# Optimization experiments

Measured on AMD Instinct MI355X. Metric: run time of the kernel, lower is better.

Reference implementation:

```python
import jax, jax.numpy as jnp
import numpy as np

# Static video grid (F, H, W); S = F*H*W tokens.
F_FRAMES, H_GRID, W_GRID = 9, 16, 28
DIM, N_HEADS = 1536, 12
HEAD_DIM = DIM // N_HEADS          # 128
ROT = HEAD_DIM // 2                # 64 complex pairs
EPS = 1e-6


def setup_inputs() -> dict:
    key = jax.random.key(0)
    ks = jax.random.split(key, 12)
    S = F_FRAMES * H_GRID * W_GRID
    scale = 0.02
    inp = {
        "x": jax.random.normal(ks[0], (1, S, DIM), jnp.float32),
        "seq_lens": jnp.array([S], jnp.int32),
        "grid_sizes": jnp.array([[F_FRAMES, H_GRID, W_GRID]], jnp.int32),
        "freqs": jax.random.normal(ks[1], (1024, ROT), jnp.float32),  # rope angles
        "Wq": jax.random.normal(ks[2], (DIM, DIM), jnp.float32) * scale,
        "bq": jnp.zeros((DIM,), jnp.float32),
        "Wk": jax.random.normal(ks[3], (DIM, DIM), jnp.float32) * scale,
        "bk": jnp.zeros((DIM,), jnp.float32),
        "Wv": jax.random.normal(ks[4], (DIM, DIM), jnp.float32) * scale,
        "bv": jnp.zeros((DIM,), jnp.float32),
        "Wo": jax.random.normal(ks[5], (DIM, DIM), jnp.float32) * scale,
        "bo": jnp.zeros((DIM,), jnp.float32),
        "gq": jnp.ones((DIM,), jnp.float32),
        "gk": jnp.ones((DIM,), jnp.float32),
    }
    return inp


def _rms_norm(h, g):
    # WanRMSNorm: h * rsqrt(mean(h^2) + eps) * weight
    var = jnp.mean(jnp.square(h), axis=-1, keepdims=True)
    return h * jax.lax.rsqrt(var + EPS) * g


def _rope_angles(freqs):
    # Split channel dim into temporal / height / width parts.
    c = ROT
    t_dim = c - 2 * (c // 3)  # 22
    s1 = c // 3               # 21
    temporal, height, width = freqs[:, :t_dim], freqs[:, t_dim:t_dim + s1], freqs[:, t_dim + s1:]
    t_ang = jnp.repeat(temporal[:F_FRAMES], H_GRID * W_GRID, axis=0)         # [S, 22]
    h_ang = jnp.tile(jnp.repeat(height[:H_GRID], W_GRID, axis=0), (F_FRAMES, 1))  # [S, 21]
    w_ang = jnp.tile(jnp.tile(width[:W_GRID], (H_GRID, 1)), (F_FRAMES, 1))        # [S, 21]
    return jnp.concatenate([t_ang, h_ang, w_ang], axis=-1)  # [S, c]


def _rope_apply(x, ang):
    # x: [B, S, n, d] viewed as complex pairs [B, S, n, d/2, 2]
    b, s, n, d = x.shape
    xp = x.reshape(b, s, n, d // 2, 2)
    xr, xi = xp[..., 0], xp[..., 1]
    cos = jnp.cos(ang)[None, :, None, :]
    sin = jnp.sin(ang)[None, :, None, :]
    out_r = xr * cos - xi * sin
    out_i = xr * sin + xi * cos
    return jnp.stack([out_r, out_i], axis=-1).reshape(b, s, n, d)


def reference(x, seq_lens, grid_sizes, freqs, Wq, bq, Wk, bk, Wv, bv, Wo, bo, gq, gk):
    b, s, _ = x.shape
    n, d = N_HEADS, HEAD_DIM
    q = _rms_norm(x @ Wq + bq, gq).reshape(b, s, n, d)
    k = _rms_norm(x @ Wk + bk, gk).reshape(b, s, n, d)
    v = (x @ Wv + bv).reshape(b, s, n, d)

    ang = _rope_angles(freqs)  # [S, d/2]
    rq = _rope_apply(q, ang)
    rk = _rope_apply(k, ang)

    # Causal frame-block mask: query in frame i attends to kv in frames <= i.
    frame_idx = jnp.arange(s) // (H_GRID * W_GRID)
    mask = frame_idx[None, :] <= frame_idx[:, None]  # [S_q, S_k]

    scale = 1.0 / jnp.sqrt(jnp.asarray(d, x.dtype))
    scores = jnp.einsum("bqnd,bknd->bnqk", rq, rk) * scale
    scores = jnp.where(mask[None, None], scores, jnp.asarray(-1e30, scores.dtype))
    probs = jax.nn.softmax(scores, axis=-1)
    attn = jnp.einsum("bnqk,bknd->bqnd", probs, v).reshape(b, s, n * d)
    return attn @ Wo + bo
```

## Files before the change

kernel.cpp:

```cpp
#include <hip/hip_runtime.h>
#include <stdint.h>

typedef unsigned short u16;
typedef unsigned int u32;
typedef __attribute__((ext_vector_type(8))) short bf16x8;
typedef __attribute__((ext_vector_type(4))) float f32x4;

#define S_LEN 4032
#define S_PAD 4096
#define DIMC  1536
#define HD    128
#define FRAME 448

static const size_t OFF_FLAG  = 0;
static const size_t OFF_CANON = 256;
static const size_t OFF_XB    = 524288;
static const size_t OFF_WT    = OFF_XB  + 12582912;
static const size_t OFF_WOT   = OFF_WT  + 14155776;
static const size_t OFF_YQ    = OFF_WOT + 4718592;
static const size_t OFF_YK    = OFF_YQ  + 12582912;
static const size_t OFF_VT    = OFF_YK  + 12582912;
static const size_t OFF_QH    = OFF_VT  + 12582912;
static const size_t OFF_KH    = OFF_QH  + 12386304;
static const size_t OFF_AT    = OFF_KH  + 12386304;
static const size_t WS_NEED   = OFF_AT  + 12582912;

#define C_BQ 0
#define C_BO 4608
#define C_GQ 6144
#define C_GK 7680
#define C_FR 9216
#define C_TOT 74752

__device__ __forceinline__ u16 f2bf(float f) {
  union { float f; u32 u; } v; v.f = f;
  u32 u = v.u;
  u32 r = (u + 0x7fffu + ((u >> 16) & 1u)) >> 16;
  return (u16)r;
}
__device__ __forceinline__ float bf2f(u16 h) {
  union { float f; u32 u; } v; v.u = ((u32)h) << 16;
  return v.f;
}

__device__ __forceinline__ void gld_lds16(const void* g, void* l) {
  __builtin_amdgcn_global_load_lds(
      (const __attribute__((address_space(1))) void*)(uintptr_t)g,
      (__attribute__((address_space(3))) void*)(u32)(uintptr_t)l,
      16, 0, 0);
}

__device__ __forceinline__ f32x4 mfma16(bf16x8 a, bf16x8 b, f32x4 c) {
  return __builtin_amdgcn_mfma_f32_16x16x32_bf16(a, b, c, 0, 0, 0);
}

__global__ void prep_all(const void* __restrict__ x,
                         const void* Wq, const void* Wk, const void* Wv, const void* Wo,
                         const void* bq, const void* bk, const void* bv, const void* bo,
                         const void* gq, const void* gk, const void* fr,
                         float* __restrict__ canon, u16* __restrict__ xb,
                         u16* __restrict__ wqkvt, u16* __restrict__ wot,
                         int* __restrict__ flag) {
  __shared__ int cnt;
  __shared__ float tile[32][33];
  const int tid = threadIdx.x;
  if (tid == 0) cnt = 0;
  __syncthreads();
  int e = (((const u16*)x)[2 * tid] >> 7) & 0xff;
  if (e > 150) atomicAdd(&cnt, 1);
  __syncthreads();
  const int fl = (cnt >= 8) ? 1 : 0;
  const int bid = blockIdx.x;
  if (bid == 0 && tid == 0) *flag = fl;

  if (bid < 9216) {
    const int z = bid / 2304;
    const int rem = bid % 2304;
    const int by = rem / 48, bx = rem % 48;
    const void* W = (z == 0) ? Wq : (z == 1) ? Wk : (z == 2) ? Wv : Wo;
    u16* dst = (z < 3) ? (wqkvt + (size_t)z * DIMC * DIMC) : wot;
    const int tx = tid & 31, ty = tid >> 5;
    const int c = bx * 32 + tx;
    #pragma unroll
    for (int i = 0; i < 4; i++) {
      int r = by * 32 + ty + i * 8;
      float v = fl ? ((const float*)W)[(size_t)r * DIMC + c]
                   : bf2f(((const u16*)W)[(size_t)r * DIMC + c]);
      tile[ty + i * 8][tx] = v;
    }
    __syncthreads();
    const int k = by * 32 + tx;
    #pragma unroll
    for (int i = 0; i < 4; i++) {
      int n = bx * 32 + ty + i * 8;
      dst[(size_t)n * DIMC + k] = f2bf(tile[tx][ty + i * 8]);
    }
  } else if (bid < 12288) {
    int i = (bid - 9216) * 256 + tid;
    if (i < (S_PAD * DIMC) / 8) {
      size_t base = (size_t)i * 8;
      int row = (int)(base / DIMC);
      union { u16 h[8]; uint4 v; } u;
      if (row < S_LEN) {
        if (fl) {
          const float* xf = (const float*)x + base;
          #pragma unroll
          for (int j = 0; j < 8; j++) u.h[j] = f2bf(xf[j]);
        } else {
          const u16* xh = (const u16*)x + base;
          #pragma unroll
          for (int j = 0; j < 8; j++) u.h[j] = xh[j];
        }
      } else {
        #pragma unroll
        for (int j = 0; j < 8; j++) u.h[j] = 0;
      }
      ((uint4*)xb)[i] = u.v;
    }
  } else {
    for (int i = (bid - 12288) * 256 + tid; i < C_TOT; i += 292 * 256) {
      const void* src; int j;
      if      (i < 1536) { src = bq; j = i; }
      else if (i < 3072) { src = bk; j = i - 1536; }
      else if (i < 4608) { src = bv; j = i - 3072; }
      else if (i < 6144) { src = bo; j = i - 4608; }
      else if (i < 7680) { src = gq; j = i - 6144; }
      else if (i < 9216) { src = gk; j = i - 7680; }
      else               { src = fr; j = i - 9216; }
      canon[i] = fl ? ((const float*)src)[j] : bf2f(((const u16*)src)[j]);
    }
  }
}

template <int MODE>
__launch_bounds__(256, 4)
__global__ void gemm_bt(const u16* __restrict__ A, const u16* __restrict__ Bt,
                        const float* __restrict__ canon,
                        u16* __restrict__ Yq, u16* __restrict__ Yk, u16* __restrict__ Vt,
                        void* __restrict__ Out, const int* __restrict__ flagp) {
  const int bm0 = blockIdx.y * 128, bn0 = blockIdx.x * 128;
  const int tid = threadIdx.x, wave = tid >> 6, lane = tid & 63;
  const int wm = wave >> 1, wn = wave & 1;
  const int l15 = lane & 15, l4 = lane >> 4;
  __shared__ u16 sA[128 * 64];
  __shared__ u16 sB[128 * 64];
  f32x4 acc[4][4];
  #pragma unroll
  for (int i = 0; i < 4; i++)
    #pragma unroll
    for (int j = 0; j < 4; j++) acc[i][j] = (f32x4){0.f, 0.f, 0.f, 0.f};

  const int swc = ((lane & 7) ^ (lane >> 3)) * 8;
  const u16* Ab = A  + (size_t)(bm0 + (lane >> 3)) * DIMC + swc;
  const u16* Bb = Bt + (size_t)(bn0 + (lane >> 3)) * DIMC + swc;

  for (int kt = 0; kt < DIMC; kt += 64) {
    __syncthreads();
    #pragma unroll
    for (int c = 0; c < 4; c++) {
      int g = wave * 4 + c;
      gld_lds16(Ab + (size_t)g * 8 * DIMC + kt, (char*)sA + g * 1024);
      gld_lds16(Bb + (size_t)g * 8 * DIMC + kt, (char*)sB + g * 1024);
    }
    __syncthreads();
    #pragma unroll
    for (int ks = 0; ks < 2; ks++) {
      bf16x8 av[4], bvv[4];
      #pragma unroll
      for (int mt = 0; mt < 4; mt++)
        av[mt]  = *(const bf16x8*)(sA + (wm * 64 + mt * 16 + l15) * 64 +
                                   (((ks * 4 + l4) ^ (l15 & 7)) * 8));
      #pragma unroll
      for (int nt = 0; nt < 4; nt++)
        bvv[nt] = *(const bf16x8*)(sB + (wn * 64 + nt * 16 + l15) * 64 +
                                   (((ks * 4 + l4) ^ (l15 & 7)) * 8));
      #pragma unroll
      for (int mt = 0; mt < 4; mt++)
        #pragma unroll
        for (int nt = 0; nt < 4; nt++)
          acc[mt][nt] = mfma16(av[mt], bvv[nt], acc[mt][nt]);
    }
  }

  const int gm0 = bm0 + wm * 64;
  const int gn0 = bn0 + wn * 64;
  if (MODE == 0) {
    #pragma unroll
    for (int nt = 0; nt < 4; nt++) {
      int gn = gn0 + nt * 16 + l15;
      float b = canon[C_BQ + gn];
      #pragma unroll
      for (int mt = 0; mt < 4; mt++) {
        int gm = gm0 + mt * 16 + l4 * 4;
        if (gn < 1536) {
          #pragma unroll
          for (int r = 0; r < 4; r++)
            Yq[(size_t)(gm + r) * DIMC + gn] = f2bf(acc[mt][nt][r] + b);
        } else if (gn < 3072) {
          int g2 = gn - 1536;
          #pragma unroll
          for (int r = 0; r < 4; r++)
            Yk[(size_t)(gm + r) * DIMC + g2] = f2bf(acc[mt][nt][r] + b);
        } else {
          int g2 = gn - 3072;
          u32 lo = (u32)f2bf(acc[mt][nt][0] + b) | ((u32)f2bf(acc[mt][nt][1] + b) << 16);
          u32 hi = (u32)f2bf(acc[mt][nt][2] + b) | ((u32)f2bf(acc[mt][nt][3] + b) << 16);
          uint2 pk; pk.x = lo; pk.y = hi;
          *(uint2*)(Vt + (size_t)g2 * S_PAD + gm) = pk;
        }
      }
    }
  } else {
    const int fl = *flagp;
    #pragma unroll
    for (int nt = 0; nt < 4; nt++) {
      int gn = gn0 + nt * 16 + l15;
      float b = canon[C_BO + gn];
      #pragma unroll
      for (int mt = 0; mt < 4; mt++) {
        int gm = gm0 + mt * 16 + l4 * 4;
        #pragma unroll
        for (int r = 0; r < 4; r++) {
          int gr = gm + r;
          if (gr < S_LEN) {
            float v = acc[mt][nt][r] + b;
            if (fl) ((float*)Out)[(size_t)gr * DIMC + gn] = v;
            else    ((u16*)Out)[(size_t)gr * DIMC + gn] = f2bf(v);
          }
        }
      }
    }
  }
}

__global__ void norm_rope(const u16* __restrict__ Yq, const u16* __restrict__ Yk,
                          const float* __restrict__ canon, u16* __restrict__ Qh,
                          u16* __restrict__ Kh) {
  const int tid = threadIdx.x, wave = tid >> 6, lane = tid & 63;
  const int s = blockIdx.x * 4 + wave;
  const int isq = (blockIdx.y == 0);
  const u16* Y = isq ? Yq : Yk;
  const float* g = canon + (isq ? C_GQ : C_GK);
  u16* Oh = isq ? Qh : Kh;
  const float sc = isq ? (0.08838834764831845f * 1.4426950408889634f) : 1.0f;

  const u32* yrow = (const u32*)Y + (size_t)s * 768;
  float xr[12], xi[12];
  float ss = 0.f;
  #pragma unroll
  for (int i = 0; i < 12; i++) {
    u32 d = yrow[lane + 64 * i];
    float a = bf2f((u16)(d & 0xffff));
    float b = bf2f((u16)(d >> 16));
    xr[i] = a; xi[i] = b;
    ss += a * a + b * b;
  }
  #pragma unroll
  for (int dd = 1; dd < 64; dd <<= 1) ss += __shfl_xor(ss, dd, 64);
  float rms = rsqrtf(ss * (1.f / 1536.f) + 1e-6f);

  int f_ = s / FRAME, hh = (s % FRAME) / 28, ww = s % 28;
  const float* fr = canon + C_FR;
  float a = (lane < 22) ? fr[f_ * 64 + lane]
          : (lane < 43) ? fr[hh * 64 + lane]
                        : fr[ww * 64 + lane];
  float si, co;
  __sincosf(a, &si, &co);

  const float2* g2 = (const float2*)g;
  #pragma unroll
  for (int i = 0; i < 12; i++) {
    int p = lane + 64 * i;
    float2 gg = g2[p];
    float r  = xr[i] * rms * gg.x;
    float im = xi[i] * rms * gg.y;
    u32 pk = (u32)f2bf((r * co - im * si) * sc) | ((u32)f2bf((r * si + im * co) * sc) << 16);
    ((u32*)Oh)[((size_t)i * S_LEN + s) * 64 + lane] = pk;
  }
}

__launch_bounds__(256, 4)
__global__ void attn_v7(const u16* __restrict__ Qh, const u16* __restrict__ Kh,
                        const u16* __restrict__ Vt, u16* __restrict__ Ab) {
  const int tid = threadIdx.x, wave = tid >> 6, lane = tid & 63;
  const int l15 = lane & 15, l4 = lane >> 4;
  const int h = blockIdx.x % 12;
  const int qb = 62 - (blockIdx.x / 12);
  const int q0 = qb * 64;
  const int nkv = (q0 / FRAME + 1) * 7;
  __shared__ u16 sK[8192];
  __shared__ u16 sV[8192];
  __shared__ u16 sP[4][1024];

  int koff[4], voff[4];
  #pragma unroll
  for (int i = 0; i < 4; i++) {
    int c = i * 256 + tid;
    int r = c >> 4, cc = (c & 15) ^ (r & 15);
    koff[i] = r * HD + cc * 8;
    int rv = c >> 3, cv = (c & 7) ^ (rv & 7);
    voff[i] = rv * S_PAD + cv * 8;
  }

  bf16x8 qf[4];
  {
    const u16* qp = Qh + ((size_t)h * S_LEN + q0 + wave * 16 + l15) * HD + l4 * 8;
    #pragma unroll
    for (int ks = 0; ks < 4; ks++) qf[ks] = *(const bf16x8*)(qp + ks * 32);
  }
  f32x4 o[8];
  #pragma unroll
  for (int i = 0; i < 8; i++) o[i] = (f32x4){0.f, 0.f, 0.f, 0.f};
  float l_i = 0.f;

  const u16* kb0 = Kh + (size_t)h * S_LEN * HD;
  const u16* vb0 = Vt + (size_t)h * HD * S_PAD;

  for (int t = 0; t < nkv; ++t) {
    __syncthreads();
    const u16* kb = kb0 + (size_t)t * 64 * HD;
    const u16* vb = vb0 + t * 64;
    #pragma unroll
    for (int i = 0; i < 4; i++) {
      int c = i * 256 + tid;
      gld_lds16(kb + koff[i], (char*)sK + (size_t)(c - lane) * 16);
      gld_lds16(vb + voff[i], (char*)sV + (size_t)(c - lane) * 16);
    }
    __syncthreads();

    f32x4 sT[4];
    #pragma unroll
    for (int nt = 0; nt < 4; nt++) sT[nt] = (f32x4){0.f, 0.f, 0.f, 0.f};
    __builtin_amdgcn_s_setprio(1);
    #pragma unroll
    for (int ks = 0; ks < 4; ks++) {
      bf16x8 kf[4];
      #pragma unroll
      for (int nt = 0; nt < 4; nt++)
        kf[nt] = *(const bf16x8*)(sK + (nt * 16 + l15) * HD + (((ks * 4 + l4) ^ l15) * 8));
      #pragma unroll
      for (int nt = 0; nt < 4; nt++)
        sT[nt] = mfma16(kf[nt], qf[ks], sT[nt]);
    }
    __builtin_amdgcn_s_setprio(0);

    float rs = 0.f;
    u16* pw = sP[wave];
    #pragma unroll
    for (int nt = 0; nt < 4; nt++) {
      #pragma unroll
      for (int r = 0; r < 4; r++) {
        float p = __builtin_amdgcn_exp2f(sT[nt][r]);
        sT[nt][r] = p; rs += p;
      }
      u32 lo = (u32)f2bf(sT[nt][0]) | ((u32)f2bf(sT[nt][1]) << 16);
      u32 hi = (u32)f2bf(sT[nt][2]) | ((u32)f2bf(sT[nt][3]) << 16);
      u32 off = (u32)((nt >> 1) * 512 + ((nt & 1) * 2 + (l4 >> 1)) * 128 + l15 * 8 + (l4 & 1) * 4);
      uint2 pk; pk.x = lo; pk.y = hi;
      *(uint2*)(pw + off) = pk;
    }
    l_i += rs;

    #pragma unroll
    for (int ks2 = 0; ks2 < 2; ks2++) {
      bf16x8 pb = *(const bf16x8*)(sP[wave] + ks2 * 512 + lane * 8);
      __builtin_amdgcn_s_setprio(1);
      #pragma unroll
      for (int vt = 0; vt < 8; vt++) {
        bf16x8 vf = *(const bf16x8*)(sV + (vt * 16 + l15) * 64 + (((ks2 * 4 + l4) ^ (l15 & 7)) * 8));
        o[vt] = mfma16(vf, pb, o[vt]);
      }
      __builtin_amdgcn_s_setprio(0);
    }
  }

  l_i += __shfl_xor(l_i, 16, 64);
  l_i += __shfl_xor(l_i, 32, 64);
  float inv = 1.f / l_i;
  const size_t orow = (size_t)(q0 + wave * 16 + l15) * DIMC + (size_t)h * HD;
  #pragma unroll
  for (int vt = 0; vt < 8; vt++) {
    u32 lo = (u32)f2bf(o[vt][0] * inv) | ((u32)f2bf(o[vt][1] * inv) << 16);
    u32 hi = (u32)f2bf(o[vt][2] * inv) | ((u32)f2bf(o[vt][3] * inv) << 16);
    uint2 pk; pk.x = lo; pk.y = hi;
    *(uint2*)(Ab + orow + vt * 16 + l4 * 4) = pk;
  }
}

extern "C" void kernel_launch(void* const* d_in, const int* in_sizes, int n_in,
                              void* d_out, int out_size, void* d_ws, size_t ws_size,
                              hipStream_t stream) {
  if (ws_size < WS_NEED) return;
  char* ws = (char*)d_ws;
  int*   flag  = (int*)(ws + OFF_FLAG);
  float* canon = (float*)(ws + OFF_CANON);
  u16* xb    = (u16*)(ws + OFF_XB);
  u16* wqkvt = (u16*)(ws + OFF_WT);
  u16* wot   = (u16*)(ws + OFF_WOT);
  u16* yq    = (u16*)(ws + OFF_YQ);
  u16* yk    = (u16*)(ws + OFF_YK);
  u16* vt    = (u16*)(ws + OFF_VT);
  u16* qh    = (u16*)(ws + OFF_QH);
  u16* kh    = (u16*)(ws + OFF_KH);
  u16* ab    = (u16*)(ws + OFF_AT);

  const void* x  = d_in[0];
  const void* fr = d_in[3];
  const void* Wq = d_in[4];  const void* bq = d_in[5];
  const void* Wk = d_in[6];  const void* bk = d_in[7];
  const void* Wv = d_in[8];  const void* bv = d_in[9];
  const void* Wo = d_in[10]; const void* bo = d_in[11];
  const void* gq = d_in[12]; const void* gk = d_in[13];

  prep_all<<<12580, 256, 0, stream>>>(x, Wq, Wk, Wv, Wo, bq, bk, bv, bo, gq, gk, fr,
                                      canon, xb, wqkvt, wot, flag);
  gemm_bt<0><<<dim3(36, 32), 256, 0, stream>>>(xb, wqkvt, canon, yq, yk, vt, nullptr, flag);
  norm_rope<<<dim3(1008, 2), 256, 0, stream>>>(yq, yk, canon, qh, kh);
  attn_v7<<<756, 256, 0, stream>>>(qh, kh, vt, ab);
  gemm_bt<1><<<dim3(12, 32), 256, 0, stream>>>(ab, wot, canon, nullptr, nullptr, nullptr, d_out, flag);
}
```

Before: 339.7 us.

## Double-buffer K/V tiles and split attention waves across query and key halves

The attention kernel now double-buffers K and V in shared memory, issuing the next tile's global-to-LDS loads before computing on the current one. This removes one barrier per iteration and overlaps loads with compute. Waves are rearranged into a 2x2 grid: each wave handles 32 query rows and half of the 64-key tile, so every loaded K/V fragment feeds two MFMAs. Partial outputs and row sums are combined through shared memory at the end. The costs are twice the LDS footprint, more accumulator registers (launch bounds lowered to 2 blocks), and an extra reduction step.

```diff
diff --git a/kernel.cpp b/kernel.cpp
--- a/kernel.cpp
+++ b/kernel.cpp
@@ -279,18 +279,20 @@
   }
 }
 
-__launch_bounds__(256, 4)
-__global__ void attn_v7(const u16* __restrict__ Qh, const u16* __restrict__ Kh,
+__launch_bounds__(256, 2)
+__global__ void attn_v8(const u16* __restrict__ Qh, const u16* __restrict__ Kh,
                         const u16* __restrict__ Vt, u16* __restrict__ Ab) {
   const int tid = threadIdx.x, wave = tid >> 6, lane = tid & 63;
   const int l15 = lane & 15, l4 = lane >> 4;
+  const int qh = wave >> 1;
+  const int kh = wave & 1;
   const int h = blockIdx.x % 12;
   const int qb = 62 - (blockIdx.x / 12);
   const int q0 = qb * 64;
   const int nkv = (q0 / FRAME + 1) * 7;
-  __shared__ u16 sK[8192];
-  __shared__ u16 sV[8192];
-  __shared__ u16 sP[4][1024];
+  __shared__ u16 sK[2][8192];
+  __shared__ u16 sV[2][8192];
+  __shared__ u16 sP[4][2][512];
 
   int koff[4], voff[4];
   #pragma unroll
@@ -302,88 +304,139 @@
     voff[i] = rv * S_PAD + cv * 8;
   }
 
-  bf16x8 qf[4];
+  bf16x8 qf[4][2];
   {
-    const u16* qp = Qh + ((size_t)h * S_LEN + q0 + wave * 16 + l15) * HD + l4 * 8;
-    #pragma unroll
-    for (int ks = 0; ks < 4; ks++) qf[ks] = *(const bf16x8*)(qp + ks * 32);
-  }
-  f32x4 o[8];
-  #pragma unroll
-  for (int i = 0; i < 8; i++) o[i] = (f32x4){0.f, 0.f, 0.f, 0.f};
-  float l_i = 0.f;
+    const u16* qp = Qh + ((size_t)h * S_LEN + q0 + qh * 32 + l15) * HD + l4 * 8;
+    #pragma unroll
+    for (int f = 0; f < 2; f++)
+      #pragma unroll
+      for (int ks = 0; ks < 4; ks++)
+        qf[ks][f] = *(const bf16x8*)(qp + f * 16 * HD + ks * 32);
+  }
+  f32x4 o[8][2];
+  #pragma unroll
+  for (int i = 0; i < 8; i++)
+    #pragma unroll
+    for (int f = 0; f < 2; f++) o[i][f] = (f32x4){0.f, 0.f, 0.f, 0.f};
+  float l_i[2] = {0.f, 0.f};
 
   const u16* kb0 = Kh + (size_t)h * S_LEN * HD;
   const u16* vb0 = Vt + (size_t)h * HD * S_PAD;
 
+  #pragma unroll
+  for (int i = 0; i < 4; i++) {
+    gld_lds16(kb0 + koff[i], (char*)sK[0] + i * 4096 + wave * 1024);
+    gld_lds16(vb0 + voff[i], (char*)sV[0] + i * 4096 + wave * 1024);
+  }
+  __syncthreads();
+
   for (int t = 0; t < nkv; ++t) {
+    const int cur = t & 1;
+    if (t + 1 < nkv) {
+      const u16* kb = kb0 + (size_t)(t + 1) * 64 * HD;
+      const u16* vb = vb0 + (t + 1) * 64;
+      #pragma unroll
+      for (int i = 0; i < 4; i++) {
+        gld_lds16(kb + koff[i], (char*)sK[cur ^ 1] + i * 4096 + wave * 1024);
+        gld_lds16(vb + voff[i], (char*)sV[cur ^ 1] + i * 4096 + wave * 1024);
+      }
+    }
+
+    f32x4 sT[2][2];
+    #pragma unroll
+    for (int nt = 0; nt < 2; nt++)
+      #pragma unroll
+      for (int f = 0; f < 2; f++) sT[nt][f] = (f32x4){0.f, 0.f, 0.f, 0.f};
+    __builtin_amdgcn_s_setprio(1);
+    #pragma unroll
+    for (int ks = 0; ks < 4; ks++) {
+      bf16x8 kf[2];
+      #pragma unroll
+      for (int nt = 0; nt < 2; nt++)
+        kf[nt] = *(const bf16x8*)(sK[cur] + (kh * 32 + nt * 16 + l15) * HD +
+                                  (((ks * 4 + l4) ^ l15) * 8));
+      #pragma unroll
+      for (int nt = 0; nt < 2; nt++)
+        #pragma unroll
+        for (int f = 0; f < 2; f++)
+          sT[nt][f] = mfma16(kf[nt], qf[ks][f], sT[nt][f]);
+    }
+    __builtin_amdgcn_s_setprio(0);
+
+    #pragma unroll
+    for (int f = 0; f < 2; f++) {
+      float rs = 0.f;
+      u16* pw = sP[wave][f];
+      #pragma unroll
+      for (int nt = 0; nt < 2; nt++) {
+        #pragma unroll
+        for (int r = 0; r < 4; r++) {
+          float p = __builtin_amdgcn_exp2f(sT[nt][f][r]);
+          sT[nt][f][r] = p; rs += p;
+        }
+        u32 lo = (u32)f2bf(sT[nt][f][0]) | ((u32)f2bf(sT[nt][f][1]) << 16);
+        u32 hi = (u32)f2bf(sT[nt][f][2]) | ((u32)f2bf(sT[nt][f][3]) << 16);
+        u32 off = (u32)((nt * 2 + (l4 >> 1)) * 128 + l15 * 8 + (l4 & 1) * 4);
+        uint2 pk; pk.x = lo; pk.y = hi;
+        *(uint2*)(pw + off) = pk;
+      }
+      l_i[f] += rs;
+    }
+
+    bf16x8 pb[2];
+    #pragma unroll
+    for (int f = 0; f < 2; f++)
+      pb[f] = *(const bf16x8*)(sP[wave][f] + lane * 8);
+    __builtin_amdgcn_s_setprio(1);
+    #pragma unroll
+    for (int vt = 0; vt < 8; vt++) {
+      bf16x8 vf = *(const bf16x8*)(sV[cur] + (vt * 16 + l15) * 64 +
+                                   (((kh * 4 + l4) ^ (l15 & 7)) * 8));
+      #pragma unroll
+      for (int f = 0; f < 2; f++)
+        o[vt][f] = mfma16(vf, pb[f], o[vt][f]);
+    }
+    __builtin_amdgcn_s_setprio(0);
+
     __syncthreads();
-    const u16* kb = kb0 + (size_t)t * 64 * HD;
-    const u16* vb = vb0 + t * 64;
-    #pragma unroll
-    for (int i = 0; i < 4; i++) {
-      int c = i * 256 + tid;
-      gld_lds16(kb + koff[i], (char*)sK + (size_t)(c - lane) * 16);
-      gld_lds16(vb + voff[i], (char*)sV + (size_t)(c - lane) * 16);
-    }
-    __syncthreads();
-
-    f32x4 sT[4];
-    #pragma unroll
-    for (int nt = 0; nt < 4; nt++) sT[nt] = (f32x4){0.f, 0.f, 0.f, 0.f};
-    __builtin_amdgcn_s_setprio(1);
-    #pragma unroll
-    for (int ks = 0; ks < 4; ks++) {
-      bf16x8 kf[4];
-      #pragma unroll
-      for (int nt = 0; nt < 4; nt++)
-        kf[nt] = *(const bf16x8*)(sK + (nt * 16 + l15) * HD + (((ks * 4 + l4) ^ l15) * 8));
-      #pragma unroll
-      for (int nt = 0; nt < 4; nt++)
-        sT[nt] = mfma16(kf[nt], qf[ks], sT[nt]);
-    }
-    __builtin_amdgcn_s_setprio(0);
-
-    float rs = 0.f;
-    u16* pw = sP[wave];
-    #pragma unroll
-    for (int nt = 0; nt < 4; nt++) {
-      #pragma unroll
-      for (int r = 0; r < 4; r++) {
-        float p = __builtin_amdgcn_exp2f(sT[nt][r]);
-        sT[nt][r] = p; rs += p;
-      }
-      u32 lo = (u32)f2bf(sT[nt][0]) | ((u32)f2bf(sT[nt][1]) << 16);
-      u32 hi = (u32)f2bf(sT[nt][2]) | ((u32)f2bf(sT[nt][3]) << 16);
-      u32 off = (u32)((nt >> 1) * 512 + ((nt & 1) * 2 + (l4 >> 1)) * 128 + l15 * 8 + (l4 & 1) * 4);
-      uint2 pk; pk.x = lo; pk.y = hi;
-      *(uint2*)(pw + off) = pk;
-    }
-    l_i += rs;
-
-    #pragma unroll
-    for (int ks2 = 0; ks2 < 2; ks2++) {
-      bf16x8 pb = *(const bf16x8*)(sP[wave] + ks2 * 512 + lane * 8);
-      __builtin_amdgcn_s_setprio(1);
+  }
+
+  #pragma unroll
+  for (int f = 0; f < 2; f++) {
+    l_i[f] += __shfl_xor(l_i[f], 16, 64);
+    l_i[f] += __shfl_xor(l_i[f], 32, 64);
+  }
+  float* mb = (float*)sK;
+  float* lb = (float*)sP;
+  if (kh == 1) {
+    #pragma unroll
+    for (int f = 0; f < 2; f++) {
+      #pragma unroll
+      for (int vt = 0; vt < 8; vt++)
+        *(f32x4*)(mb + qh * 4096 + (f * 8 + vt) * 256 + lane * 4) = o[vt][f];
+      lb[qh * 128 + f * 64 + lane] = l_i[f];
+    }
+  }
+  __syncthreads();
+  if (kh == 0) {
+    #pragma unroll
+    for (int f = 0; f < 2; f++) {
+      float l = l_i[f] + lb[qh * 128 + f * 64 + lane];
+      float inv = 1.f / l;
+      const size_t orow = (size_t)(q0 + qh * 32 + f * 16 + l15) * DIMC + (size_t)h * HD;
       #pragma unroll
       for (int vt = 0; vt < 8; vt++) {
-        bf16x8 vf = *(const bf16x8*)(sV + (vt * 16 + l15) * 64 + (((ks2 * 4 + l4) ^ (l15 & 7)) * 8));
-        o[vt] = mfma16(vf, pb, o[vt]);
-      }
-      __builtin_amdgcn_s_setprio(0);
-    }
-  }
-
-  l_i += __shfl_xor(l_i, 16, 64);
-  l_i += __shfl_xor(l_i, 32, 64);
-  float inv = 1.f / l_i;
-  const size_t orow = (size_t)(q0 + wave * 16 + l15) * DIMC + (size_t)h * HD;
-  #pragma unroll
-  for (int vt = 0; vt < 8; vt++) {
-    u32 lo = (u32)f2bf(o[vt][0] * inv) | ((u32)f2bf(o[vt][1] * inv) << 16);
-    u32 hi = (u32)f2bf(o[vt][2] * inv) | ((u32)f2bf(o[vt][3] * inv) << 16);
-    uint2 pk; pk.x = lo; pk.y = hi;
-    *(uint2*)(Ab + orow + vt * 16 + l4 * 4) = pk;
+        f32x4 op = *(const f32x4*)(mb + qh * 4096 + (f * 8 + vt) * 256 + lane * 4);
+        float o0 = (o[vt][f][0] + op[0]) * inv;
+        float o1 = (o[vt][f][1] + op[1]) * inv;
+        float o2 = (o[vt][f][2] + op[2]) * inv;
+        float o3 = (o[vt][f][3] + op[3]) * inv;
+        u32 lo = (u32)f2bf(o0) | ((u32)f2bf(o1) << 16);
+        u32 hi = (u32)f2bf(o2) | ((u32)f2bf(o3) << 16);
+        uint2 pk; pk.x = lo; pk.y = hi;
+        *(uint2*)(Ab + orow + vt * 16 + l4 * 4) = pk;
+      }
+    }
   }
 }
 
@@ -416,6 +469,6 @@
                                       canon, xb, wqkvt, wot, flag);
   gemm_bt<0><<<dim3(36, 32), 256, 0, stream>>>(xb, wqkvt, canon, yq, yk, vt, nullptr, flag);
   norm_rope<<<dim3(1008, 2), 256, 0, stream>>>(yq, yk, canon, qh, kh);
-  attn_v7<<<756, 256, 0, stream>>>(qh, kh, vt, ab);
+  attn_v8<<<756, 256, 0, stream>>>(qh, kh, vt, ab);
   gemm_bt<1><<<dim3(12, 32), 256, 0, stream>>>(ab, wot, canon, nullptr, nullptr, nullptr, d_out, flag);
 }
```

Result: faster. 323.9 us (-4.7%).
